# Optimization experiments

Measured on AMD Instinct MI355X. Metric: run time of the kernel, lower is better.

## Reference

```python
import jax, jax.numpy as jnp
import numpy as np

BN_EPS = 1e-5


def setup_inputs() -> dict:
    key = jax.random.key(0)
    k1, k2, k3 = jax.random.split(key, 3)
    N, C_in, T, V = 32, 64, 288, 25
    C_out = 64
    fv = jax.random.normal(k1, (N, C_in, T, V), dtype=jnp.float32)
    adj = jax.random.uniform(k2, (V, V), dtype=jnp.float32)
    # Conv2d(2*C_in, C_out, 1x1) weight flattened to [C_out, 2*C_in]; kaiming-ish scale
    W = jax.random.normal(k3, (C_out, 2 * C_in), dtype=jnp.float32) * (2.0 / (2 * C_in)) ** 0.5
    b = jnp.zeros((C_out,), dtype=jnp.float32)
    gamma = jnp.ones((C_out,), dtype=jnp.float32)   # bn_init scale=1
    beta = jnp.zeros((C_out,), dtype=jnp.float32)
    return {"fv": fv, "adj": adj, "W": W, "b": b, "gamma": gamma, "beta": beta}


def reference(fv, adj, W, b, gamma, beta):
    # fv: [N, C, T, V]; neighbor aggregation over joints via learnable adjacency
    fv_agg = jnp.einsum('nctv,vy->ncty', fv, adj)
    cat = jnp.concatenate([fv, fv_agg], axis=1)            # [N, 2C, T, V]
    # 1x1 conv == channel matmul
    out = jnp.einsum('ncty,oc->noty', cat, W) + b[None, :, None, None]
    # BatchNorm2d in training mode: batch stats over (N, T, V) per channel
    mean = out.mean(axis=(0, 2, 3), keepdims=True)
    var = out.var(axis=(0, 2, 3), keepdims=True)
    out = (out - mean) * jax.lax.rsqrt(var + BN_EPS)
    out = out * gamma[None, :, None, None] + beta[None, :, None, None]
    return jax.nn.relu(out)
```

## Files before the change

### kernel.cpp

```cpp
#include <hip/hip_runtime.h>

#define N_DIM 32
#define C_IN 64
#define C_OUT 64
#define T_DIM 288
#define V_DIM 25
#define TV 7200
#define NTV 230400
#define TOTAL 14745600
#define BN_EPS 1e-5f

#define WS_WINT 0
#define WS_SUM 8192
#define WS_SQ  8256

__global__ __launch_bounds__(256) void prep_kernel(const float* __restrict__ W,
                                                   float* __restrict__ ws) {
  const int tid = threadIdx.x;
  if (tid < 128) ws[WS_SUM + tid] = 0.0f;
  for (int i = tid; i < 8192; i += 256) {
    const int s = i & 1;
    const int oo = (i >> 1) & 31;
    const int c = (i >> 6) & 63;
    const int h = i >> 12;
    const int o = h * 32 + oo;
    ws[WS_WINT + i] = W[o * 128 + s * 64 + c];
  }
}

__device__ __forceinline__ float reduce32_lane(float* v, int lane) {
#pragma unroll
  for (int s = 0; s < 5; ++s) {
    const int m = 1 << s;
    const bool up = (lane & m) != 0;
    const int pairs = 32 >> (s + 1);
#pragma unroll
    for (int q = 0; q < pairs; ++q) {
      const float keep = up ? v[2 * q + 1] : v[2 * q];
      const float send = up ? v[2 * q] : v[2 * q + 1];
      const float recv = __shfl_xor(send, m, 64);
      v[q] = keep + recv;
    }
  }
  return v[0];
}

__global__ __launch_bounds__(256) void main_kernel(const float* __restrict__ fv,
                                                   const float* __restrict__ adj,
                                                   const float* __restrict__ wint,
                                                   float* __restrict__ stats,
                                                   float* __restrict__ out) {
  __shared__ float lsum[C_OUT];
  __shared__ float lsq[C_OUT];
  const int tid = threadIdx.x;
  if (tid < 64) lsum[tid] = 0.0f;
  else if (tid < 128) lsq[tid - 64] = 0.0f;
  __syncthreads();

  const int half = __builtin_amdgcn_readfirstlane(tid) >> 7;
  const int col = (blockIdx.x << 7) + (tid & 127);
  const int lane = tid & 63;

  const int n = col / TV;
  const int r = col - n * TV;
  const int t = r / V_DIM;
  const int y = r - t * V_DIM;

  float adjcol[V_DIM];
#pragma unroll
  for (int v = 0; v < V_DIM; ++v) adjcol[v] = adj[v * V_DIM + y];

  const float* base = fv + (size_t)n * (C_IN * TV) + t * V_DIM;
  const float* __restrict__ wbase = wint + half * 4096;

  float acc[32];
#pragma unroll
  for (int oo = 0; oo < 32; ++oo) acc[oo] = 0.0f;

  for (int c = 0; c < C_IN; ++c) {
    const float* p = base + c * TV;
    const float x = p[y];
    float xa0 = 0.f, xa1 = 0.f, xa2 = 0.f, xa3 = 0.f;
#pragma unroll
    for (int v = 0; v < 24; v += 4) {
      xa0 = fmaf(p[v + 0], adjcol[v + 0], xa0);
      xa1 = fmaf(p[v + 1], adjcol[v + 1], xa1);
      xa2 = fmaf(p[v + 2], adjcol[v + 2], xa2);
      xa3 = fmaf(p[v + 3], adjcol[v + 3], xa3);
    }
    xa0 = fmaf(p[24], adjcol[24], xa0);
    const float xa = (xa0 + xa1) + (xa2 + xa3);

    const float* __restrict__ w = wbase + c * 64;
#pragma unroll
    for (int oo = 0; oo < 32; ++oo)
      acc[oo] = fmaf(x, w[oo * 2], fmaf(xa, w[oo * 2 + 1], acc[oo]));
  }

  float* op = out + (size_t)n * (C_OUT * TV) + (size_t)(half * 32) * TV
              + t * V_DIM + y;
#pragma unroll
  for (int oo = 0; oo < 32; ++oo) op[oo * TV] = acc[oo];

  float sq[32];
#pragma unroll
  for (int i = 0; i < 32; ++i) sq[i] = acc[i] * acc[i];
  float s = reduce32_lane(acc, lane);
  s += __shfl_xor(s, 32, 64);
  float q = reduce32_lane(sq, lane);
  q += __shfl_xor(q, 32, 64);

  if (lane < 32) {
    atomicAdd(&lsum[half * 32 + lane], s);
    atomicAdd(&lsq[half * 32 + lane], q);
  }
  __syncthreads();
  if (tid < 64) {
    atomicAdd(&stats[tid], lsum[tid]);
    atomicAdd(&stats[64 + tid], lsq[tid]);
  }
}

__global__ __launch_bounds__(256) void bn_kernel(const float* __restrict__ stats,
                                                 const float* __restrict__ gamma,
                                                 const float* __restrict__ beta,
                                                 float* __restrict__ out) {
  __shared__ float s_scale[C_OUT];
  __shared__ float s_shift[C_OUT];
  const int tid = threadIdx.x;
  if (tid < C_OUT) {
    const float inv = 1.0f / (float)NTV;
    const float mean = stats[tid] * inv;
    const float var = fmaf(stats[64 + tid], inv, -mean * mean);
    const float sc = gamma[tid] * rsqrtf(var + BN_EPS);
    s_scale[tid] = sc;
    s_shift[tid] = fmaf(-mean, sc, beta[tid]);
  }
  __syncthreads();

  float4* o4 = reinterpret_cast<float4*>(out);
  const int total4 = TOTAL / 4;
  const int stride = gridDim.x * blockDim.x;
  for (int i = blockIdx.x * blockDim.x + tid; i < total4; i += stride) {
    float4 v = o4[i];
    const int o = (i / 1800) & 63;
    const float sc = s_scale[o];
    const float sh = s_shift[o];
    v.x = fmaxf(fmaf(v.x, sc, sh), 0.0f);
    v.y = fmaxf(fmaf(v.y, sc, sh), 0.0f);
    v.z = fmaxf(fmaf(v.z, sc, sh), 0.0f);
    v.w = fmaxf(fmaf(v.w, sc, sh), 0.0f);
    o4[i] = v;
  }
}

extern "C" void kernel_launch(void* const* d_in, const int* in_sizes, int n_in,
                              void* d_out, int out_size, void* d_ws, size_t ws_size,
                              hipStream_t stream) {
  const float* fv = (const float*)d_in[0];
  const float* adj = (const float*)d_in[1];
  const float* W = (const float*)d_in[2];
  const float* gamma = (const float*)d_in[4];
  const float* beta = (const float*)d_in[5];
  float* out = (float*)d_out;
  float* ws = (float*)d_ws;

  hipLaunchKernelGGL(prep_kernel, dim3(1), dim3(256), 0, stream, W, ws);
  hipLaunchKernelGGL(main_kernel, dim3(NTV / 128), dim3(256), 0, stream,
                     fv, adj, ws + WS_WINT, ws + WS_SUM, out);
  hipLaunchKernelGGL(bn_kernel, dim3(2048), dim3(256), 0, stream,
                     ws + WS_SUM, gamma, beta, out);
}
```

Measured before the change: 259.7 us.

## Stage fv rows through double-buffered LDS with register prefetch in main kernel

The main kernel now loads each block's fv rows for one channel into a double-buffered shared-memory tile, with a two-channel register prefetch pipeline. Threads read the row and its neighbour sum as float4 from LDS instead of issuing 25 redundant global loads per channel. The prep kernel is spread across 32 blocks and launch bounds request higher occupancy. In exchange there is a __syncthreads on every channel iteration and only 175 staging threads, which could serialise latency.

```diff
diff --git a/kernel.cpp b/kernel.cpp
--- a/kernel.cpp
+++ b/kernel.cpp
@@ -6,9 +6,11 @@
 #define T_DIM 288
 #define V_DIM 25
 #define TV 7200
+#define NROWS 9216
 #define NTV 230400
 #define TOTAL 14745600
 #define BN_EPS 1e-5f
+#define NTILES 1800
 
 #define WS_WINT 0
 #define WS_SUM 8192
@@ -16,16 +18,14 @@
 
 __global__ __launch_bounds__(256) void prep_kernel(const float* __restrict__ W,
                                                    float* __restrict__ ws) {
-  const int tid = threadIdx.x;
-  if (tid < 128) ws[WS_SUM + tid] = 0.0f;
-  for (int i = tid; i < 8192; i += 256) {
-    const int s = i & 1;
-    const int oo = (i >> 1) & 31;
-    const int c = (i >> 6) & 63;
-    const int h = i >> 12;
-    const int o = h * 32 + oo;
-    ws[WS_WINT + i] = W[o * 128 + s * 64 + c];
-  }
+  const int i = blockIdx.x * 256 + threadIdx.x;
+  if (blockIdx.x == 0 && threadIdx.x < 128) ws[WS_SUM + threadIdx.x] = 0.0f;
+  const int s = i & 1;
+  const int oo = (i >> 1) & 31;
+  const int c = (i >> 6) & 63;
+  const int h = i >> 12;
+  const int o = h * 32 + oo;
+  ws[WS_WINT + i] = W[o * 128 + s * 64 + c];
 }
 
 __device__ __forceinline__ float reduce32_lane(float* v, int lane) {
@@ -45,50 +45,73 @@
   return v[0];
 }
 
-__global__ __launch_bounds__(256) void main_kernel(const float* __restrict__ fv,
-                                                   const float* __restrict__ adj,
-                                                   const float* __restrict__ wint,
-                                                   float* __restrict__ stats,
-                                                   float* __restrict__ out) {
+__global__ __launch_bounds__(256, 4) void main_kernel(
+    const float* __restrict__ fv, const float* __restrict__ adj,
+    const float* __restrict__ wint, float* __restrict__ stats,
+    float* __restrict__ out) {
+  __shared__ __align__(16) float buf[2][7][36];
   __shared__ float lsum[C_OUT];
   __shared__ float lsq[C_OUT];
+
   const int tid = threadIdx.x;
-  if (tid < 64) lsum[tid] = 0.0f;
-  else if (tid < 128) lsq[tid - 64] = 0.0f;
-  __syncthreads();
+  if (tid < 64) { lsum[tid] = 0.0f; lsq[tid] = 0.0f; }
 
   const int half = __builtin_amdgcn_readfirstlane(tid) >> 7;
-  const int col = (blockIdx.x << 7) + (tid & 127);
   const int lane = tid & 63;
+  const float* __restrict__ wbase = wint + half * 4096;
 
-  const int n = col / TV;
-  const int r = col - n * TV;
-  const int t = r / V_DIM;
-  const int y = r - t * V_DIM;
+  const int j0 = blockIdx.x << 7;
+  const int col = j0 + (tid & 127);
+  const int row = col / V_DIM;
+  const int y = col - row * V_DIM;
+  const int rbase = j0 / V_DIM;
+  const int rowoff = row - rbase;
 
   float adjcol[V_DIM];
 #pragma unroll
   for (int v = 0; v < V_DIM; ++v) adjcol[v] = adj[v * V_DIM + y];
 
-  const float* base = fv + (size_t)n * (C_IN * TV) + t * V_DIM;
-  const float* __restrict__ wbase = wint + half * 4096;
+  bool stager = false;
+  int base_e = 0, srr = 0, sv = 0;
+  if (tid < 175) {
+    srr = tid / V_DIM;
+    sv = tid - srr * V_DIM;
+    const int Rg = rbase + srr;
+    if (Rg < NROWS) {
+      stager = true;
+      const int n = Rg / T_DIM;
+      const int t = Rg - n * T_DIM;
+      base_e = n * (C_IN * TV) + t * V_DIM + sv;
+    }
+  }
 
   float acc[32];
 #pragma unroll
   for (int oo = 0; oo < 32; ++oo) acc[oo] = 0.0f;
 
+  float r0 = stager ? fv[base_e] : 0.0f;
+  float r1 = stager ? fv[base_e + TV] : 0.0f;
+
+#pragma unroll 1
   for (int c = 0; c < C_IN; ++c) {
-    const float* p = base + c * TV;
-    const float x = p[y];
+    if (tid < 175) buf[c & 1][srr][sv] = r0;
+    r0 = r1;
+    if (stager && c + 2 < C_IN) r1 = fv[base_e + (c + 2) * TV];
+    __syncthreads();
+
+    const float* __restrict__ br = &buf[c & 1][rowoff][0];
+    const float x = br[y];
+    const float4* __restrict__ b4 = reinterpret_cast<const float4*>(br);
     float xa0 = 0.f, xa1 = 0.f, xa2 = 0.f, xa3 = 0.f;
 #pragma unroll
-    for (int v = 0; v < 24; v += 4) {
-      xa0 = fmaf(p[v + 0], adjcol[v + 0], xa0);
-      xa1 = fmaf(p[v + 1], adjcol[v + 1], xa1);
-      xa2 = fmaf(p[v + 2], adjcol[v + 2], xa2);
-      xa3 = fmaf(p[v + 3], adjcol[v + 3], xa3);
+    for (int q = 0; q < 6; ++q) {
+      const float4 f = b4[q];
+      xa0 = fmaf(f.x, adjcol[4 * q + 0], xa0);
+      xa1 = fmaf(f.y, adjcol[4 * q + 1], xa1);
+      xa2 = fmaf(f.z, adjcol[4 * q + 2], xa2);
+      xa3 = fmaf(f.w, adjcol[4 * q + 3], xa3);
     }
-    xa0 = fmaf(p[24], adjcol[24], xa0);
+    xa0 = fmaf(br[24], adjcol[24], xa0);
     const float xa = (xa0 + xa1) + (xa2 + xa3);
 
     const float* __restrict__ w = wbase + c * 64;
@@ -97,10 +120,13 @@
       acc[oo] = fmaf(x, w[oo * 2], fmaf(xa, w[oo * 2 + 1], acc[oo]));
   }
 
-  float* op = out + (size_t)n * (C_OUT * TV) + (size_t)(half * 32) * TV
-              + t * V_DIM + y;
+  {
+    const int n = row / T_DIM;
+    const int t = row - n * T_DIM;
+    float* op = out + ((size_t)n * C_OUT + half * 32) * TV + t * V_DIM + y;
 #pragma unroll
-  for (int oo = 0; oo < 32; ++oo) op[oo * TV] = acc[oo];
+    for (int oo = 0; oo < 32; ++oo) op[oo * TV] = acc[oo];
+  }
 
   float sq[32];
 #pragma unroll
@@ -165,8 +191,8 @@
   float* out = (float*)d_out;
   float* ws = (float*)d_ws;
 
-  hipLaunchKernelGGL(prep_kernel, dim3(1), dim3(256), 0, stream, W, ws);
-  hipLaunchKernelGGL(main_kernel, dim3(NTV / 128), dim3(256), 0, stream,
+  hipLaunchKernelGGL(prep_kernel, dim3(32), dim3(256), 0, stream, W, ws);
+  hipLaunchKernelGGL(main_kernel, dim3(NTILES), dim3(256), 0, stream,
                      fv, adj, ws + WS_WINT, ws + WS_SUM, out);
   hipLaunchKernelGGL(bn_kernel, dim3(2048), dim3(256), 0, stream,
                      ws + WS_SUM, gamma, beta, out);
```

After: 298.3 us. 14.9% more time.

## Split adjacency aggregation into separate kernel staging results in output buffer

Applied to the files above, without the earlier changes.

The joint aggregation fv·adj moves into its own kernel, which writes the aggregated features into the output buffer as scratch. The conv kernel then reads x and xa as plain coalesced loads instead of recomputing 25-tap dot products per channel. It adds a launch-bounds occupancy hint and a barrier before overwriting the scratch. The prep and BN kernels are also reshaped so that each BN block handles one (n,o) plane with a scalar scale and shift. The cost is an extra full-size write and read of the intermediate (about 59 MB each way) in exchange for less redundant ALU and scattered-load work.

```diff
diff --git a/kernel.cpp b/kernel.cpp
--- a/kernel.cpp
+++ b/kernel.cpp
@@ -9,6 +9,7 @@
 #define NTV 230400
 #define TOTAL 14745600
 #define BN_EPS 1e-5f
+#define NTILES 1800
 
 #define WS_WINT 0
 #define WS_SUM 8192
@@ -16,16 +17,33 @@
 
 __global__ __launch_bounds__(256) void prep_kernel(const float* __restrict__ W,
                                                    float* __restrict__ ws) {
-  const int tid = threadIdx.x;
-  if (tid < 128) ws[WS_SUM + tid] = 0.0f;
-  for (int i = tid; i < 8192; i += 256) {
-    const int s = i & 1;
-    const int oo = (i >> 1) & 31;
-    const int c = (i >> 6) & 63;
-    const int h = i >> 12;
-    const int o = h * 32 + oo;
-    ws[WS_WINT + i] = W[o * 128 + s * 64 + c];
+  const int i = blockIdx.x * 256 + threadIdx.x;
+  if (blockIdx.x == 0 && threadIdx.x < 128) ws[WS_SUM + threadIdx.x] = 0.0f;
+  const int s = i & 1;
+  const int oo = (i >> 1) & 31;
+  const int c = (i >> 6) & 63;
+  const int h = i >> 12;
+  const int o = h * 32 + oo;
+  ws[WS_WINT + i] = W[o * 128 + s * 64 + c];
+}
+
+__global__ __launch_bounds__(256) void agg_kernel(const float* __restrict__ fv,
+                                                  const float* __restrict__ adj,
+                                                  float* __restrict__ aggout) {
+  const int e = blockIdx.x * 256 + threadIdx.x;
+  const int r = e / V_DIM;
+  const int y = e - r * V_DIM;
+  const float* __restrict__ p = fv + r * V_DIM;
+  float a0 = 0.f, a1 = 0.f, a2 = 0.f, a3 = 0.f;
+#pragma unroll
+  for (int v = 0; v < 24; v += 4) {
+    a0 = fmaf(p[v + 0], adj[(v + 0) * V_DIM + y], a0);
+    a1 = fmaf(p[v + 1], adj[(v + 1) * V_DIM + y], a1);
+    a2 = fmaf(p[v + 2], adj[(v + 2) * V_DIM + y], a2);
+    a3 = fmaf(p[v + 3], adj[(v + 3) * V_DIM + y], a3);
   }
+  a0 = fmaf(p[24], adj[24 * V_DIM + y], a0);
+  aggout[e] = (a0 + a1) + (a2 + a3);
 }
 
 __device__ __forceinline__ float reduce32_lane(float* v, int lane) {
@@ -45,60 +63,41 @@
   return v[0];
 }
 
-__global__ __launch_bounds__(256) void main_kernel(const float* __restrict__ fv,
-                                                   const float* __restrict__ adj,
-                                                   const float* __restrict__ wint,
-                                                   float* __restrict__ stats,
-                                                   float* __restrict__ out) {
+__global__ __launch_bounds__(256, 6) void conv_kernel(
+    const float* __restrict__ fv, const float* __restrict__ wint,
+    float* __restrict__ stats, float* __restrict__ out) {
   __shared__ float lsum[C_OUT];
   __shared__ float lsq[C_OUT];
   const int tid = threadIdx.x;
-  if (tid < 64) lsum[tid] = 0.0f;
-  else if (tid < 128) lsq[tid - 64] = 0.0f;
+  if (tid < 64) { lsum[tid] = 0.0f; lsq[tid] = 0.0f; }
   __syncthreads();
 
   const int half = __builtin_amdgcn_readfirstlane(tid) >> 7;
-  const int col = (blockIdx.x << 7) + (tid & 127);
   const int lane = tid & 63;
+  const float* __restrict__ wbase = wint + half * 4096;
 
-  const int n = col / TV;
-  const int r = col - n * TV;
-  const int t = r / V_DIM;
-  const int y = r - t * V_DIM;
-
-  float adjcol[V_DIM];
-#pragma unroll
-  for (int v = 0; v < V_DIM; ++v) adjcol[v] = adj[v * V_DIM + y];
-
-  const float* base = fv + (size_t)n * (C_IN * TV) + t * V_DIM;
-  const float* __restrict__ wbase = wint + half * 4096;
+  const int j = (blockIdx.x << 7) + (tid & 127);
+  const int n = j / TV;
+  const int rem = j - n * TV;
+  const int base = n * (C_IN * TV) + rem;
 
   float acc[32];
 #pragma unroll
   for (int oo = 0; oo < 32; ++oo) acc[oo] = 0.0f;
 
+#pragma unroll 4
   for (int c = 0; c < C_IN; ++c) {
-    const float* p = base + c * TV;
-    const float x = p[y];
-    float xa0 = 0.f, xa1 = 0.f, xa2 = 0.f, xa3 = 0.f;
-#pragma unroll
-    for (int v = 0; v < 24; v += 4) {
-      xa0 = fmaf(p[v + 0], adjcol[v + 0], xa0);
-      xa1 = fmaf(p[v + 1], adjcol[v + 1], xa1);
-      xa2 = fmaf(p[v + 2], adjcol[v + 2], xa2);
-      xa3 = fmaf(p[v + 3], adjcol[v + 3], xa3);
-    }
-    xa0 = fmaf(p[24], adjcol[24], xa0);
-    const float xa = (xa0 + xa1) + (xa2 + xa3);
-
+    const float x = fv[base + c * TV];
+    const float xa = out[base + c * TV];
     const float* __restrict__ w = wbase + c * 64;
 #pragma unroll
     for (int oo = 0; oo < 32; ++oo)
       acc[oo] = fmaf(x, w[oo * 2], fmaf(xa, w[oo * 2 + 1], acc[oo]));
   }
 
-  float* op = out + (size_t)n * (C_OUT * TV) + (size_t)(half * 32) * TV
-              + t * V_DIM + y;
+  __syncthreads();
+
+  float* op = out + base + (size_t)(half * 32) * TV;
 #pragma unroll
   for (int oo = 0; oo < 32; ++oo) op[oo * TV] = acc[oo];
 
@@ -125,32 +124,22 @@
                                                  const float* __restrict__ gamma,
                                                  const float* __restrict__ beta,
                                                  float* __restrict__ out) {
-  __shared__ float s_scale[C_OUT];
-  __shared__ float s_shift[C_OUT];
-  const int tid = threadIdx.x;
-  if (tid < C_OUT) {
-    const float inv = 1.0f / (float)NTV;
-    const float mean = stats[tid] * inv;
-    const float var = fmaf(stats[64 + tid], inv, -mean * mean);
-    const float sc = gamma[tid] * rsqrtf(var + BN_EPS);
-    s_scale[tid] = sc;
-    s_shift[tid] = fmaf(-mean, sc, beta[tid]);
-  }
-  __syncthreads();
+  const int o = blockIdx.x & 63;
+  const float inv = 1.0f / (float)NTV;
+  const float mean = stats[o] * inv;
+  const float var = fmaf(stats[64 + o], inv, -mean * mean);
+  const float sc = gamma[o] * rsqrtf(var + BN_EPS);
+  const float sh = fmaf(-mean, sc, beta[o]);
 
-  float4* o4 = reinterpret_cast<float4*>(out);
-  const int total4 = TOTAL / 4;
-  const int stride = gridDim.x * blockDim.x;
-  for (int i = blockIdx.x * blockDim.x + tid; i < total4; i += stride) {
-    float4 v = o4[i];
-    const int o = (i / 1800) & 63;
-    const float sc = s_scale[o];
-    const float sh = s_shift[o];
+  float4* base = reinterpret_cast<float4*>(out) + (size_t)blockIdx.x * 1800;
+#pragma unroll 1
+  for (int i = threadIdx.x; i < 1800; i += 256) {
+    float4 v = base[i];
     v.x = fmaxf(fmaf(v.x, sc, sh), 0.0f);
     v.y = fmaxf(fmaf(v.y, sc, sh), 0.0f);
     v.z = fmaxf(fmaf(v.z, sc, sh), 0.0f);
     v.w = fmaxf(fmaf(v.w, sc, sh), 0.0f);
-    o4[i] = v;
+    base[i] = v;
   }
 }
 
@@ -165,9 +154,11 @@
   float* out = (float*)d_out;
   float* ws = (float*)d_ws;
 
-  hipLaunchKernelGGL(prep_kernel, dim3(1), dim3(256), 0, stream, W, ws);
-  hipLaunchKernelGGL(main_kernel, dim3(NTV / 128), dim3(256), 0, stream,
-                     fv, adj, ws + WS_WINT, ws + WS_SUM, out);
-  hipLaunchKernelGGL(bn_kernel, dim3(2048), dim3(256), 0, stream,
+  hipLaunchKernelGGL(prep_kernel, dim3(32), dim3(256), 0, stream, W, ws);
+  hipLaunchKernelGGL(agg_kernel, dim3(TOTAL / 256), dim3(256), 0, stream,
+                     fv, adj, out);
+  hipLaunchKernelGGL(conv_kernel, dim3(NTILES), dim3(256), 0, stream,
+                     fv, ws + WS_WINT, ws + WS_SUM, out);
+  hipLaunchKernelGGL(bn_kernel, dim3(N_DIM * C_OUT), dim3(256), 0, stream,
                      ws + WS_SUM, gamma, beta, out);
 }
```

After: 353.2 us. 1.36x slower.
